# Kernel tuning notes

Measured on AMD Instinct MI355X. Metric: run time of the kernel, lower is better.

## Reference

```python
import jax, jax.numpy as jnp
import numpy as np

H = 1024            # hinges
S = 4               # shims
N = H + 2           # nodes
NC = 2 * N          # flattened DOFs
B = 256             # batch of independent chains
L = 1.0             # rest edge length
DT = 0.001          # integration step
GAMMA = 2.0         # damping
N_STEPS = 64        # relaxation steps (truncated scan)


def setup_inputs() -> dict:
    key = jax.random.key(0)
    k1, k2, k3, k4, k5 = jax.random.split(key, 5)
    xs = jnp.arange(N, dtype=jnp.float32) * L
    base = jnp.stack([xs, jnp.zeros(N, jnp.float32)], axis=-1)          # (N,2) straight chain
    noise = 0.01 * jax.random.normal(k1, (B, N, 2), jnp.float32)
    noise = noise.at[:, :2, :].set(0.0)                                  # nodes 0,1 fixed exactly
    pos0 = base[None] + noise                                            # (B,N,2)
    tip_base = base[-1]
    tip_off = jnp.stack([-0.1 * L * H * jax.random.uniform(k2, (B,)),
                         2.0 * jax.random.normal(k3, (B,))], axis=-1)
    tip_pos = (tip_base[None] + tip_off).astype(jnp.float32)             # (B,2) imposed tip
    thetas_ss = 0.3 * jax.random.uniform(k4, (H,), jnp.float32)          # snap-through angles
    buckle_arr = jax.random.randint(k5, (H, S), 0, 2).astype(jnp.int32)  # {0,1} -> maps to {-1,+1}
    return dict(pos0=pos0, tip_pos=tip_pos, thetas_ss=thetas_ss, buckle_arr=buckle_arr,
                k_stiff=jnp.float32(10.0), k_soft=jnp.float32(0.5), k_stretch=jnp.float32(1000.0))


def _free_mask():
    m = np.ones(NC, bool)
    m[:4] = False            # nodes 0,1 fixed (dof_idx = 2*node+comp)
    m[2 * (N - 1):] = False  # tip node imposed
    return jnp.asarray(m)


def _energy(x, thetas_ss, buckle_pm, k_stiff, k_soft, k_stretch):
    """Total potential energy of one chain; x is flattened (NC,)."""
    pos = x.reshape(N, 2)
    v1 = pos[1:-1] - pos[:-2]                 # (H,2) edge into hinge h
    v2 = pos[2:] - pos[1:-1]                  # (H,2) edge out of hinge h
    theta = jnp.arctan2(v1[:, 0] * v2[:, 1] - v1[:, 1] * v2[:, 0],
                        jnp.sum(v1 * v2, -1))               # (H,) CCW hinge angle
    d = pos[1:] - pos[:-1]
    elen = jnp.sqrt(jnp.sum(d * d, -1))                     # (H+1,) edge lengths
    T = theta[:, None]                                      # (H,1)
    TH = thetas_ss[:, None]                                 # (H,1)
    stiff = ((buckle_pm == 1) & (T < TH)) | ((buckle_pm == -1) & (T > -TH))  # (H,S)
    k_rot = jnp.where(stiff, k_stiff, k_soft)
    e_rot = 0.5 * jnp.sum(k_rot * (T - TH) ** 2)
    e_str = 0.5 * jnp.sum(k_stretch * (elen - L) ** 2)
    return e_rot + e_str


def reference(pos0, tip_pos, thetas_ss, buckle_arr, k_stiff, k_soft, k_stretch):
    buckle_pm = 2 * buckle_arr - 1                           # {0,1} -> {-1,+1}
    free = _free_mask()                                      # (NC,) static
    x0 = pos0.reshape(B, NC)
    x0 = x0.at[:, 2 * (N - 1)].set(tip_pos[:, 0]).at[:, 2 * (N - 1) + 1].set(tip_pos[:, 1])
    v0 = jnp.zeros_like(x0)

    grad_e = jax.vmap(jax.grad(
        lambda x: _energy(x, thetas_ss, buckle_pm, k_stiff, k_soft, k_stretch)))

    def step(carry, _):
        x, v = carry
        f = -grad_e(x)                                       # potential force, (B,NC)
        v = jnp.where(free[None], v + DT * (f - GAMMA * v), 0.0)
        x = jnp.where(free[None], x + DT * v, x)             # fixed/imposed DOFs held
        return (x, v), None

    (xf, _vf), _ = jax.lax.scan(step, (x0, v0), None, length=N_STEPS)
    return xf                                                # (B,NC) relaxed positions
```

## Files before the change

### kernel.cpp

```cpp
#include <hip/hip_runtime.h>

#define NN 1026
#define NE 1025
#define NA 1024
#define BLK 1024

__device__ __forceinline__ float fast_atan2f(float y, float x) {
    float ax = __builtin_fabsf(x), ay = __builtin_fabsf(y);
    float mx = fmaxf(ax, ay), mn = fminf(ax, ay);
    float a  = mn * __builtin_amdgcn_rcpf(mx);
    float s  = a * a;
    float r  = fmaf(s, -0.0117212f,  0.05265332f);
    r = fmaf(s, r, -0.11643287f);
    r = fmaf(s, r,  0.19354346f);
    r = fmaf(s, r, -0.33262347f);
    r = fmaf(s, r,  0.99997726f);
    r *= a;
    if (ay > ax)  r = 1.57079637f - r;
    if (x < 0.0f) r = 3.14159274f - r;
    return copysignf(r, y);
}

__global__ __launch_bounds__(BLK)
void equil_kernel(const float* __restrict__ pos0,
                  const float* __restrict__ tip_pos,
                  const float* __restrict__ thetas_ss,
                  const int*   __restrict__ buckle,
                  const float* __restrict__ kstiff_p,
                  const float* __restrict__ ksoft_p,
                  const float* __restrict__ kstretch_p,
                  float* __restrict__ out)
{
    __shared__ float2 pos[NN];
    __shared__ float2 Ps[NE];
    __shared__ float2 Qs[NA];

    const int b   = blockIdx.x;
    const int t   = threadIdx.x;
    const float k_str  = kstretch_p[0];
    const float k_sd   = kstiff_p[0] - ksoft_p[0];
    const float k4soft = 4.0f * ksoft_p[0];

    const float2* p0 = (const float2*)(pos0 + (size_t)b * NN * 2);
    float2 myp;
    if (t < 1023) {
        myp = p0[t + 2];
    } else {
        myp.x = tip_pos[2*b];  myp.y = tip_pos[2*b+1];
    }
    pos[t + 2] = myp;
    if (t < 2) pos[t] = p0[t];

    const float TH = thetas_ss[t];
    const int4 bk  = ((const int4*)buckle)[t];
    const float npl = (float)(bk.x + bk.y + bk.z + bk.w);
    float2 vel = make_float2(0.f, 0.f);
    __syncthreads();

    for (int s = 0; s < 64; ++s) {
        float2 pa = pos[t], pb = pos[t+1];
        float v1x = pb.x - pa.x,  v1y = pb.y - pa.y;
        float v2x = myp.x - pb.x, v2y = myp.y - pb.y;
        float l2a = fmaf(v1x, v1x, v1y * v1y);
        float l2b = fmaf(v2x, v2x, v2y * v2y);
        float cr  = v1x * v2y - v1y * v2x;
        float dt_ = fmaf(v1x, v2x, v1y * v2y);
        float theta = fast_atan2f(cr, dt_);
        float cnt = (theta <  TH ? npl        : 0.f)
                  + (theta > -TH ? 4.f - npl  : 0.f);
        float K = fmaf(cnt, k_sd, k4soft);
        float m = K * (theta - TH);
        float ila = __builtin_amdgcn_rsqf(l2a);
        float ilb = __builtin_amdgcn_rsqf(l2b);
        float m1 = m * ila * ila;
        float m2 = m * ilb * ilb;
        float2 Bv; Bv.x = -m2 * v2y;  Bv.y =  m2 * v2x;
        float sca = k_str * (1.0f - ila);
        float2 P;  P.x = fmaf(sca, v1x,  m1 * v1y);
                   P.y = fmaf(sca, v1y, -m1 * v1x);
        float2 Q;  Q.x = P.x - Bv.x;  Q.y = P.y - Bv.y;
        Ps[t] = P;
        Qs[t] = Q;
        if (t == NA - 1) {
            float scb = k_str * (1.0f - ilb);
            float2 PN; PN.x = scb * v2x; PN.y = scb * v2y;
            Ps[NA] = PN;
        }
        __syncthreads();

        if (t < 1023) {
            float2 Pn = Ps[t+2];
            float2 Qm = Qs[t+1];
            float fx = Pn.x - Qm.x - Bv.x;
            float fy = Pn.y - Qm.y - Bv.y;
            vel.x += 0.001f * (fx - 2.0f * vel.x);
            vel.y += 0.001f * (fy - 2.0f * vel.y);
            myp.x += 0.001f * vel.x;
            myp.y += 0.001f * vel.y;
            pos[t + 2] = myp;
        }
        __syncthreads();
    }

    float2* o = (float2*)(out + (size_t)b * NN * 2);
    o[t + 2] = myp;
    if (t < 2) o[t] = pos[t];
}

extern "C" void kernel_launch(void* const* d_in, const int* in_sizes, int n_in,
                              void* d_out, int out_size, void* d_ws, size_t ws_size,
                              hipStream_t stream) {
    const float* pos0   = (const float*)d_in[0];
    const float* tip    = (const float*)d_in[1];
    const float* thetas = (const float*)d_in[2];
    const int*   buckle = (const int*)  d_in[3];
    const float* ks     = (const float*)d_in[4];
    const float* ko     = (const float*)d_in[5];
    const float* kr     = (const float*)d_in[6];
    float* out = (float*)d_out;
    hipLaunchKernelGGL(equil_kernel, dim3(256), dim3(BLK), 0, stream,
                       pos0, tip, thetas, buckle, ks, ko, kr, out);
}
```

Measured before the change: 46.05 us.

## Replicate node state per thread and double-buffer to halve barriers per step

Each thread now keeps its own copies of the three nodes its hinge touches (positions and velocities) and integrates all three redundantly. Neighbouring force terms come from one shared float4 buffer, and the kernel alternates between two buffers. This removes the second __syncthreads per step and the shared position array, leaving one barrier per step. The cost is triple integration work, more registers, and four float4 shared reads per step. Redundant copies must stay bitwise consistent across threads, which holds because every thread applies the same arithmetic.

```diff
diff --git a/kernel.cpp b/kernel.cpp
--- a/kernel.cpp
+++ b/kernel.cpp
@@ -1,9 +1,7 @@
 #include <hip/hip_runtime.h>
 
-#define NN 1026
-#define NE 1025
-#define NA 1024
 #define BLK 1024
+#define NSLOT 1028
 
 __device__ __forceinline__ float fast_atan2f(float y, float x) {
     float ax = __builtin_fabsf(x), ay = __builtin_fabsf(y);
@@ -21,6 +19,15 @@
     return copysignf(r, y);
 }
 
+__device__ __forceinline__ void integ(float2& p, float2& v, float fx, float fy) {
+    float tx = fmaf(-2.0f, v.x, fx);
+    float ty = fmaf(-2.0f, v.y, fy);
+    v.x = fmaf(0.001f, tx, v.x);
+    v.y = fmaf(0.001f, ty, v.y);
+    p.x = fmaf(0.001f, v.x, p.x);
+    p.y = fmaf(0.001f, v.y, p.y);
+}
+
 __global__ __launch_bounds__(BLK)
 void equil_kernel(const float* __restrict__ pos0,
                   const float* __restrict__ tip_pos,
@@ -31,80 +38,85 @@
                   const float* __restrict__ kstretch_p,
                   float* __restrict__ out)
 {
-    __shared__ float2 pos[NN];
-    __shared__ float2 Ps[NE];
-    __shared__ float2 Qs[NA];
+    __shared__ float4 PB0[NSLOT];
+    __shared__ float4 PB1[NSLOT];
 
-    const int b   = blockIdx.x;
-    const int t   = threadIdx.x;
+    const int b = blockIdx.x;
+    const int t = threadIdx.x;
     const float k_str  = kstretch_p[0];
     const float k_sd   = kstiff_p[0] - ksoft_p[0];
     const float k4soft = 4.0f * ksoft_p[0];
 
-    const float2* p0 = (const float2*)(pos0 + (size_t)b * NN * 2);
-    float2 myp;
-    if (t < 1023) {
-        myp = p0[t + 2];
-    } else {
-        myp.x = tip_pos[2*b];  myp.y = tip_pos[2*b+1];
-    }
-    pos[t + 2] = myp;
-    if (t < 2) pos[t] = p0[t];
+    const float2* p0g = (const float2*)(pos0 + (size_t)b * 2052);
+    float2 pA = p0g[t];
+    float2 pB = p0g[t + 1];
+    float2 pC;
+    if (t < 1023) pC = p0g[t + 2];
+    else { pC.x = tip_pos[2*b]; pC.y = tip_pos[2*b+1]; }
 
     const float TH = thetas_ss[t];
     const int4 bk  = ((const int4*)buckle)[t];
     const float npl = (float)(bk.x + bk.y + bk.z + bk.w);
-    float2 vel = make_float2(0.f, 0.f);
-    __syncthreads();
+    float2 vA = make_float2(0.f,0.f), vB = vA, vC = vA;
 
-    for (int s = 0; s < 64; ++s) {
-        float2 pa = pos[t], pb = pos[t+1];
-        float v1x = pb.x - pa.x,  v1y = pb.y - pa.y;
-        float v2x = myp.x - pb.x, v2y = myp.y - pb.y;
-        float l2a = fmaf(v1x, v1x, v1y * v1y);
-        float l2b = fmaf(v2x, v2x, v2y * v2y);
-        float cr  = v1x * v2y - v1y * v2x;
-        float dt_ = fmaf(v1x, v2x, v1y * v2y);
-        float theta = fast_atan2f(cr, dt_);
-        float cnt = (theta <  TH ? npl        : 0.f)
-                  + (theta > -TH ? 4.f - npl  : 0.f);
-        float K = fmaf(cnt, k_sd, k4soft);
-        float m = K * (theta - TH);
-        float ila = __builtin_amdgcn_rsqf(l2a);
-        float ilb = __builtin_amdgcn_rsqf(l2b);
-        float m1 = m * ila * ila;
-        float m2 = m * ilb * ilb;
-        float2 Bv; Bv.x = -m2 * v2y;  Bv.y =  m2 * v2x;
-        float sca = k_str * (1.0f - ila);
-        float2 P;  P.x = fmaf(sca, v1x,  m1 * v1y);
-                   P.y = fmaf(sca, v1y, -m1 * v1x);
-        float2 Q;  Q.x = P.x - Bv.x;  Q.y = P.y - Bv.y;
-        Ps[t] = P;
-        Qs[t] = Q;
-        if (t == NA - 1) {
-            float scb = k_str * (1.0f - ilb);
-            float2 PN; PN.x = scb * v2x; PN.y = scb * v2y;
-            Ps[NA] = PN;
-        }
-        __syncthreads();
+    const bool updA = (t >= 2);
+    const bool updB = (t >= 1);
+    const bool updC = (t <= 1022);
 
-        if (t < 1023) {
-            float2 Pn = Ps[t+2];
-            float2 Qm = Qs[t+1];
-            float fx = Pn.x - Qm.x - Bv.x;
-            float fy = Pn.y - Qm.y - Bv.y;
-            vel.x += 0.001f * (fx - 2.0f * vel.x);
-            vel.y += 0.001f * (fy - 2.0f * vel.y);
-            myp.x += 0.001f * vel.x;
-            myp.y += 0.001f * vel.y;
-            pos[t + 2] = myp;
-        }
-        __syncthreads();
+    if (t < 2)   { PB0[t]    = make_float4(0,0,0,0); PB1[t]    = make_float4(0,0,0,0); }
+    if (t == 2)  { PB0[1027] = make_float4(0,0,0,0); PB1[1027] = make_float4(0,0,0,0); }
+
+#define STEP(BUF)                                                             \
+    {                                                                         \
+        float v1x = pB.x - pA.x, v1y = pB.y - pA.y;                           \
+        float v2x = pC.x - pB.x, v2y = pC.y - pB.y;                           \
+        float l2a = fmaf(v1x, v1x, v1y * v1y);                                \
+        float l2b = fmaf(v2x, v2x, v2y * v2y);                                \
+        float cr  = v1x * v2y - v1y * v2x;                                    \
+        float dt_ = fmaf(v1x, v2x, v1y * v2y);                                \
+        float theta = fast_atan2f(cr, dt_);                                   \
+        float cnt = (theta <  TH ? npl       : 0.f)                           \
+                  + (theta > -TH ? 4.f - npl : 0.f);                          \
+        float K = fmaf(cnt, k_sd, k4soft);                                    \
+        float m = K * (theta - TH);                                           \
+        float ila = __builtin_amdgcn_rsqf(l2a);                               \
+        float ilb = __builtin_amdgcn_rsqf(l2b);                               \
+        float m1 = m * ila * ila;                                             \
+        float m2 = m * ilb * ilb;                                             \
+        float Bx = -m2 * v2y, By = m2 * v2x;                                  \
+        float sca = k_str * (1.0f - ila);                                     \
+        float Px = fmaf(sca, v1x,  m1 * v1y);                                 \
+        float Py = fmaf(sca, v1y, -m1 * v1x);                                 \
+        BUF[t + 2] = make_float4(Px, Py, Bx, By);                             \
+        if (t == 1023) {                                                      \
+            float scb = k_str * (1.0f - ilb);                                 \
+            BUF[1026] = make_float4(scb * v2x, scb * v2y, 0.f, 0.f);          \
+        }                                                                     \
+        __syncthreads();                                                      \
+        float4 jm2 = BUF[t];                                       \
+        float4 jm1 = BUF[t + 1];                                   \
+        float4 jp1 = BUF[t + 3];                                   \
+        float4 jp2 = BUF[t + 4];                                   \
+        float f0x = Px    - (jm1.x - jm1.z) - jm2.z;                          \
+        float f0y = Py    - (jm1.y - jm1.w) - jm2.w;                          \
+        float f1x = jp1.x - (Px    - Bx)    - jm1.z;                          \
+        float f1y = jp1.y - (Py    - By)    - jm1.w;                          \
+        float f2x = jp2.x - (jp1.x - jp1.z) - Bx;                             \
+        float f2y = jp2.y - (jp1.y - jp1.w) - By;                             \
+        if (updA) integ(pA, vA, f0x, f0y);                                    \
+        if (updB) integ(pB, vB, f1x, f1y);                                    \
+        if (updC) integ(pC, vC, f2x, f2y);                                    \
     }
 
-    float2* o = (float2*)(out + (size_t)b * NN * 2);
-    o[t + 2] = myp;
-    if (t < 2) o[t] = pos[t];
+    for (int s = 0; s < 32; ++s) {
+        STEP(PB0);
+        STEP(PB1);
+    }
+#undef STEP
+
+    float2* o = (float2*)(out + (size_t)b * 2052);
+    o[t + 2] = pC;
+    if (t == 0) { o[0] = pA; o[1] = pB; }
 }
 
 extern "C" void kernel_launch(void* const* d_in, const int* in_sizes, int n_in,
```

Result: slower. 56.48 us (+22.6%).

## Process two hinges per thread with 512-thread blocks and packed vector math

Applied to the files above, without the earlier changes.

Halves the block size so each thread owns two consecutive nodes and their hinges. It computes three edges locally, which cuts redundant edge and rsqrt work and shared-memory traffic per node. Positions and forces move through float4 shared arrays, and the arithmetic uses 2-wide vector types that may map to packed FP32 instructions. In exchange each thread carries more registers and has a longer dependency chain per step, and parallelism per block drops.

```diff
diff --git a/kernel.cpp b/kernel.cpp
--- a/kernel.cpp
+++ b/kernel.cpp
@@ -1,9 +1,9 @@
 #include <hip/hip_runtime.h>
 
-#define NN 1026
-#define NE 1025
-#define NA 1024
-#define BLK 1024
+#define BLK 512
+typedef float v2f __attribute__((ext_vector_type(2)));
+
+__device__ __forceinline__ v2f vs(float s) { return (v2f){s, s}; }
 
 __device__ __forceinline__ float fast_atan2f(float y, float x) {
     float ax = __builtin_fabsf(x), ay = __builtin_fabsf(y);
@@ -31,80 +31,107 @@
                   const float* __restrict__ kstretch_p,
                   float* __restrict__ out)
 {
-    __shared__ float2 pos[NN];
-    __shared__ float2 Ps[NE];
-    __shared__ float2 Qs[NA];
+    __shared__ float4 Pos4[513];
+    __shared__ float4 PP4[513];
+    __shared__ float2 Q2[513];
 
-    const int b   = blockIdx.x;
-    const int t   = threadIdx.x;
+    const int b = blockIdx.x;
+    const int t = threadIdx.x;
     const float k_str  = kstretch_p[0];
     const float k_sd   = kstiff_p[0] - ksoft_p[0];
     const float k4soft = 4.0f * ksoft_p[0];
 
-    const float2* p0 = (const float2*)(pos0 + (size_t)b * NN * 2);
-    float2 myp;
-    if (t < 1023) {
-        myp = p0[t + 2];
-    } else {
-        myp.x = tip_pos[2*b];  myp.y = tip_pos[2*b+1];
-    }
-    pos[t + 2] = myp;
-    if (t < 2) pos[t] = p0[t];
+    const float2* p0g = (const float2*)(pos0 + (size_t)b * 2052);
+    float2 c0f = p0g[0], c1f = p0g[1];
+    const v2f c0 = (v2f){c0f.x, c0f.y};
+    const v2f c1 = (v2f){c1f.x, c1f.y};
 
-    const float TH = thetas_ss[t];
-    const int4 bk  = ((const int4*)buckle)[t];
-    const float npl = (float)(bk.x + bk.y + bk.z + bk.w);
-    float2 vel = make_float2(0.f, 0.f);
+    float2 a_ = p0g[2*t + 2];
+    v2f pA = (v2f){a_.x, a_.y};
+    v2f pB;
+    if (t < 511) { float2 b_ = p0g[2*t + 3]; pB = (v2f){b_.x, b_.y}; }
+    else         { pB = (v2f){tip_pos[2*b], tip_pos[2*b+1]}; }
+
+    const float2 th2 = ((const float2*)thetas_ss)[t];
+    const float TH0 = th2.x, TH1 = th2.y;
+    const int4 bk0 = ((const int4*)buckle)[2*t];
+    const int4 bk1 = ((const int4*)buckle)[2*t + 1];
+    const float npl0 = (float)(bk0.x + bk0.y + bk0.z + bk0.w);
+    const float npl1 = (float)(bk1.x + bk1.y + bk1.z + bk1.w);
+
+    v2f vA = vs(0.f), vB = vs(0.f);
+
+    Pos4[t] = make_float4(pA.x, pA.y, pB.x, pB.y);
+    if (t == 0) Q2[512] = make_float2(0.f, 0.f);
     __syncthreads();
 
     for (int s = 0; s < 64; ++s) {
-        float2 pa = pos[t], pb = pos[t+1];
-        float v1x = pb.x - pa.x,  v1y = pb.y - pa.y;
-        float v2x = myp.x - pb.x, v2y = myp.y - pb.y;
-        float l2a = fmaf(v1x, v1x, v1y * v1y);
-        float l2b = fmaf(v2x, v2x, v2y * v2y);
-        float cr  = v1x * v2y - v1y * v2x;
-        float dt_ = fmaf(v1x, v2x, v1y * v2y);
-        float theta = fast_atan2f(cr, dt_);
-        float cnt = (theta <  TH ? npl        : 0.f)
-                  + (theta > -TH ? 4.f - npl  : 0.f);
-        float K = fmaf(cnt, k_sd, k4soft);
-        float m = K * (theta - TH);
-        float ila = __builtin_amdgcn_rsqf(l2a);
-        float ilb = __builtin_amdgcn_rsqf(l2b);
-        float m1 = m * ila * ila;
-        float m2 = m * ilb * ilb;
-        float2 Bv; Bv.x = -m2 * v2y;  Bv.y =  m2 * v2x;
-        float sca = k_str * (1.0f - ila);
-        float2 P;  P.x = fmaf(sca, v1x,  m1 * v1y);
-                   P.y = fmaf(sca, v1y, -m1 * v1x);
-        float2 Q;  Q.x = P.x - Bv.x;  Q.y = P.y - Bv.y;
-        Ps[t] = P;
-        Qs[t] = Q;
-        if (t == NA - 1) {
-            float scb = k_str * (1.0f - ilb);
-            float2 PN; PN.x = scb * v2x; PN.y = scb * v2y;
-            Ps[NA] = PN;
+        float4 L = Pos4[t == 0 ? 0 : t - 1];
+        v2f nL0 = (t == 0) ? c0 : (v2f){L.x, L.y};
+        v2f nL1 = (t == 0) ? c1 : (v2f){L.z, L.w};
+        v2f e0 = nL1 - nL0;
+        v2f e1 = pA - nL1;
+        v2f e2 = pB - pA;
+        float l20 = fmaf(e0.x, e0.x, e0.y * e0.y);
+        float l21 = fmaf(e1.x, e1.x, e1.y * e1.y);
+        float l22 = fmaf(e2.x, e2.x, e2.y * e2.y);
+        float ila0 = __builtin_amdgcn_rsqf(l20);
+        float ila1 = __builtin_amdgcn_rsqf(l21);
+        float ila2 = __builtin_amdgcn_rsqf(l22);
+
+        float cr0 = e0.x * e1.y - e0.y * e1.x;
+        float dt0 = fmaf(e0.x, e1.x, e0.y * e1.y);
+        float th_0 = fast_atan2f(cr0, dt0);
+        float cnt0 = (th_0 <  TH0 ? npl0       : 0.f)
+                   + (th_0 > -TH0 ? 4.f - npl0 : 0.f);
+        float m0 = fmaf(cnt0, k_sd, k4soft) * (th_0 - TH0);
+        float cr1 = e1.x * e2.y - e1.y * e2.x;
+        float dt1 = fmaf(e1.x, e2.x, e1.y * e2.y);
+        float th_1 = fast_atan2f(cr1, dt1);
+        float cnt1 = (th_1 <  TH1 ? npl1       : 0.f)
+                   + (th_1 > -TH1 ? 4.f - npl1 : 0.f);
+        float m1 = fmaf(cnt1, k_sd, k4soft) * (th_1 - TH1);
+
+        float il20 = ila0 * ila0, il21 = ila1 * ila1, il22 = ila2 * ila2;
+        float ca0 = m0 * il20, cb0 = m0 * il21;
+        float ca1 = m1 * il21, cb1 = m1 * il22;
+        v2f rot0 = (v2f){e0.y, -e0.x};
+        v2f rot1 = (v2f){e1.y, -e1.x};
+        v2f rot2 = (v2f){e2.y, -e2.x};
+        float sc0 = k_str * (1.0f - ila0);
+        float sc1 = k_str * (1.0f - ila1);
+        v2f P0 = vs(sc0) * e0 + vs(ca0) * rot0;
+        v2f B0 = vs(-cb0) * rot1;
+        v2f Q0 = P0 - B0;
+        v2f P1 = vs(sc1) * e1 + vs(ca1) * rot1;
+        v2f B1 = vs(-cb1) * rot2;
+        v2f Q1 = P1 - B1;
+
+        PP4[t] = make_float4(P0.x, P0.y, P1.x, P1.y);
+        Q2[t]  = make_float2(Q0.x, Q0.y);
+        if (t == 511) {
+            float sc2 = k_str * (1.0f - ila2);
+            PP4[512] = make_float4(sc2 * e2.x, sc2 * e2.y, sc2 * e2.x, sc2 * e2.y);
         }
         __syncthreads();
 
-        if (t < 1023) {
-            float2 Pn = Ps[t+2];
-            float2 Qm = Qs[t+1];
-            float fx = Pn.x - Qm.x - Bv.x;
-            float fy = Pn.y - Qm.y - Bv.y;
-            vel.x += 0.001f * (fx - 2.0f * vel.x);
-            vel.y += 0.001f * (fy - 2.0f * vel.y);
-            myp.x += 0.001f * vel.x;
-            myp.y += 0.001f * vel.y;
-            pos[t + 2] = myp;
+        float4 Pn  = PP4[t + 1];
+        float2 Qn2 = Q2[t + 1];
+        v2f f0 = ((v2f){Pn.x, Pn.y} - Q1) - B0;
+        v2f f1 = ((v2f){Pn.z, Pn.w} - (v2f){Qn2.x, Qn2.y}) - B1;
+        vA = vA + vs(0.001f) * (f0 - vs(2.0f) * vA);
+        pA = pA + vs(0.001f) * vA;
+        if (t < 511) {
+            vB = vB + vs(0.001f) * (f1 - vs(2.0f) * vB);
+            pB = pB + vs(0.001f) * vB;
         }
+        Pos4[t] = make_float4(pA.x, pA.y, pB.x, pB.y);
         __syncthreads();
     }
 
-    float2* o = (float2*)(out + (size_t)b * NN * 2);
-    o[t + 2] = myp;
-    if (t < 2) o[t] = pos[t];
+    float4* o4 = (float4*)(out + (size_t)b * 2052);
+    o4[t + 1] = make_float4(pA.x, pA.y, pB.x, pB.y);
+    if (t == 0) o4[0] = make_float4(c0.x, c0.y, c1.x, c1.y);
 }
 
 extern "C" void kernel_launch(void* const* d_in, const int* in_sizes, int n_in,
```

After: 47.63 us. 3.4% more time.
